# Kernel tuning notes

Hardware: AMD Instinct MI355X
Metric: run time of the kernel (lower is better)

The kernel has to match this reference:

```python
import math
import jax, jax.numpy as jnp
import numpy as np

B, H, HKV, L, S, D = 1, 32, 8, 2048, 2048, 128
N_REP = H // HKV          # 4
SCALE = 1.0 / math.sqrt(D)


def setup_inputs() -> dict:
    key = jax.random.key(0)
    k1, k2, k3, k4 = jax.random.split(key, 4)
    query = jax.random.normal(k1, (B, H, L, D), dtype=jnp.float32)
    k_ = jax.random.normal(k2, (B, HKV, S, D), dtype=jnp.float32)
    v_ = jax.random.normal(k3, (B, HKV, S, D), dtype=jnp.float32)
    attn_mask = jax.random.normal(k4, (B, 1, L, S), dtype=jnp.float32)
    return {"query": query, "key": k_, "value": v_, "attn_mask": attn_mask}


def reference(query, key, value, attn_mask):
    # repeat_kv: Q -> [B, HKV, n_rep, L, D]; K/V stay [B, HKV, S, D]
    # (the torch code reshapes K/V to [B, HKV, 1, S, D]; broadcasting via
    # einsum is equivalent), mask unsqueezed at dim 1 -> [B, 1, 1, L, S].
    q = query.reshape(B, HKV, N_REP, L, D)
    scores = jnp.einsum("bkrld,bksd->bkrls", q, key)          # [B,HKV,n_rep,L,S]
    scores = scores + attn_mask[:, None]                        # broadcast add
    # softmax_fp8(x, dim=-1, invAttnHead=1/sqrt(D)) scales input by invAttnHead
    w = jax.nn.softmax(scores * SCALE, axis=-1)
    # dropout_p = 0.0 -> identity
    out = jnp.einsum("bkrls,bksd->bkrld", w, value)             # [B,HKV,n_rep,L,D]
    return out
```

## Files before the change

### kernel.cpp

```cpp
#include <hip/hip_runtime.h>

#define NH   32
#define NKV  8
#define LQ   2048
#define SK   2048
#define DH   128
#define BM   128
#define BN   64
#define NT   (SK / BN)
#define VSTRIDE 72

typedef __attribute__((ext_vector_type(8)))  short bf8;
typedef __attribute__((ext_vector_type(16))) float f16v;
typedef __attribute__((ext_vector_type(4)))  unsigned int u32x4;

#define CL2E 0.12754308753f

#if __has_builtin(__builtin_amdgcn_exp2f)
#define EXP2F(x) __builtin_amdgcn_exp2f(x)
#else
#define EXP2F(x) exp2f(x)
#endif

__device__ __forceinline__ unsigned short f2bf(float f) {
    unsigned int u = __builtin_bit_cast(unsigned int, f);
    u = (u + 0x7FFFu + ((u >> 16) & 1u)) >> 16;
    return (unsigned short)u;
}

__device__ __forceinline__ unsigned int cvtpk_bf16(float lo, float hi) {
    unsigned int r;
    asm("v_cvt_pk_bf16_f32 %0, %1, %2" : "=v"(r) : "v"(lo), "v"(hi));
    return r;
}

__device__ __forceinline__ float bflo(unsigned int u) {
    return __builtin_bit_cast(float, u << 16);
}
__device__ __forceinline__ float bfhi(unsigned int u) {
    return __builtin_bit_cast(float, u & 0xFFFF0000u);
}

#define GLOAD_LDS16(g, l)                                                      \
    __builtin_amdgcn_global_load_lds(                                          \
        (const __attribute__((address_space(1))) void*)(g),                    \
        (__attribute__((address_space(3))) void*)(l), 16, 0, 0)

__global__ __launch_bounds__(256) void convert_k_kernel(
    const float* __restrict__ K, unsigned short* __restrict__ Kb)
{
    unsigned int cid = blockIdx.x * 256 + threadIdx.x;
    unsigned int p   = cid & 15;
    unsigned int row = cid >> 4;
    unsigned int s   = row & (SK - 1);
    unsigned int c   = p ^ (s & 15);
    const float* src = K + (size_t)row * DH + c * 8;
    float4 a = *(const float4*)(src);
    float4 b = *(const float4*)(src + 4);
    bf8 o;
    o[0] = (short)f2bf(a.x); o[1] = (short)f2bf(a.y);
    o[2] = (short)f2bf(a.z); o[3] = (short)f2bf(a.w);
    o[4] = (short)f2bf(b.x); o[5] = (short)f2bf(b.y);
    o[6] = (short)f2bf(b.z); o[7] = (short)f2bf(b.w);
    *(bf8*)(Kb + (size_t)row * DH + p * 8) = o;
}

__global__ __launch_bounds__(256) void transpose_v_kernel(
    const float* __restrict__ V, unsigned short* __restrict__ VTb)
{
    __shared__ __align__(16) unsigned short Vl[DH * VSTRIDE];
    const int tid = threadIdx.x;
    const int kv  = blockIdx.x >> 5;
    const int t   = blockIdx.x & 31;
    const int s0  = t * 64;
    const float* Vh = V + (size_t)kv * SK * DH;

    #pragma unroll
    for (int i = 0; i < 8; ++i) {
        int idx = tid * 4 + i * 1024;
        int s = idx >> 7, d = idx & 127;
        const float4 v4 = *(const float4*)(Vh + (size_t)(s0 + s) * DH + d);
        Vl[(d + 0) * VSTRIDE + s] = f2bf(v4.x);
        Vl[(d + 1) * VSTRIDE + s] = f2bf(v4.y);
        Vl[(d + 2) * VSTRIDE + s] = f2bf(v4.z);
        Vl[(d + 3) * VSTRIDE + s] = f2bf(v4.w);
    }
    __syncthreads();
    unsigned short* out = VTb + (size_t)(kv * 32 + t) * (DH * 64);
    #pragma unroll
    for (int i = 0; i < 4; ++i) {
        int c = tid + i * 256;
        int d = c >> 3, p = c & 7;
        int sc = (p ^ (d & 7)) * 8;
        *(bf8*)(out + d * 64 + p * 8) = *(const bf8*)(Vl + d * VSTRIDE + sc);
    }
}

__global__ __launch_bounds__(256) void convert_m_kernel(
    const float* __restrict__ M, unsigned short* __restrict__ Mb)
{
    unsigned int cid = blockIdx.x * 256 + threadIdx.x;
    unsigned int row = cid >> 8;
    unsigned int l   = (cid & 255) * 8;
    unsigned int T   = l & ~63u;
    unsigned int loc = l & 63;
    unsigned int mt = loc >> 5, w = loc & 31;
    unsigned int hh = w >> 4, g0 = (w >> 2) & 3;
    const float* src = M + (size_t)row * SK + T + mt * 32 + hh * 4;
    float4 a = *(const float4*)(src + g0 * 8);
    float4 b = *(const float4*)(src + (g0 + 1) * 8);
    bf8 o;
    o[0] = (short)f2bf(a.x * CL2E); o[1] = (short)f2bf(a.y * CL2E);
    o[2] = (short)f2bf(a.z * CL2E); o[3] = (short)f2bf(a.w * CL2E);
    o[4] = (short)f2bf(b.x * CL2E); o[5] = (short)f2bf(b.y * CL2E);
    o[6] = (short)f2bf(b.z * CL2E); o[7] = (short)f2bf(b.w * CL2E);
    *(bf8*)(Mb + (size_t)row * SK + l) = o;
}

__global__ __launch_bounds__(256, 2) void fattn_kernel(
    const float* __restrict__ Q, const unsigned short* __restrict__ Kb,
    const unsigned short* __restrict__ VTb, const unsigned short* __restrict__ Mb,
    float* __restrict__ O)
{
    __shared__ __align__(1024) unsigned char smem[65536];
    unsigned char* KB = smem;
    unsigned char* VB = smem + 32768;

    const int tid  = threadIdx.x;
    const int wave = tid >> 6;
    const int lane = tid & 63;
    const int l32  = lane & 31;
    const int hh   = lane >> 5;

    const int bx = ((int)blockIdx.x & 7) * 64 + ((int)blockIdx.x >> 3);
    const int h  = bx >> 4;
    const int lt = bx & 15;
    const int q0 = lt * BM;
    const int kv = h >> 2;

    const float* Qh = Q + (size_t)h * LQ * DH;
    const unsigned char* Kg = (const unsigned char*)(Kb  + (size_t)kv * SK * DH);
    const unsigned char* Vg = (const unsigned char*)(VTb + (size_t)kv * SK * DH);

    const int qrow = q0 + wave * 32 + l32;
    const unsigned short* Mq = Mb + (size_t)qrow * SK + hh * 16;

    bf8 bQ[8];
    {
        const float* qp = Qh + (size_t)qrow * DH + hh * 8;
        #pragma unroll
        for (int ks = 0; ks < 8; ++ks) {
            float4 a = *(const float4*)(qp + ks * 16);
            float4 b = *(const float4*)(qp + ks * 16 + 4);
            bf8 o;
            o[0] = (short)f2bf(a.x); o[1] = (short)f2bf(a.y);
            o[2] = (short)f2bf(a.z); o[3] = (short)f2bf(a.w);
            o[4] = (short)f2bf(b.x); o[5] = (short)f2bf(b.y);
            o[6] = (short)f2bf(b.z); o[7] = (short)f2bf(b.w);
            bQ[ks] = o;
        }
    }

    const int krow0 = l32 * 256 + ((hh * 16) ^ ((l32 & 15) << 4));
    const int vrowz = l32 * 128 + ((hh * 16) ^ ((l32 & 7) << 4));

    const int stoff = wave * 4096 + lane * 16;

    f16v accO[4];
    #pragma unroll
    for (int dt = 0; dt < 4; ++dt)
        #pragma unroll
        for (int r = 0; r < 16; ++r) accO[dt][r] = 0.f;
    float lpart = 0.f;

    #pragma unroll
    for (int c = 0; c < 4; ++c) GLOAD_LDS16(Kg + stoff + c * 1024, KB + stoff + c * 1024);
    #pragma unroll
    for (int c = 0; c < 4; ++c) GLOAD_LDS16(Vg + stoff + c * 1024, VB + stoff + c * 1024);

    for (int t = 0; t < NT; ++t) {
        const int cur = t & 1;

        const unsigned short* mp = Mq + t * 64;
        u32x4 mA0 = *(const u32x4*)(mp);
        u32x4 mB0 = *(const u32x4*)(mp + 8);
        u32x4 mA1 = *(const u32x4*)(mp + 32);
        u32x4 mB1 = *(const u32x4*)(mp + 40);
        __builtin_amdgcn_sched_barrier(0);

        {
            const int tn = (t + 1) & (NT - 1);
            const unsigned char* ksrc = Kg + (size_t)tn * 16384 + stoff;
            const unsigned char* vsrc = Vg + (size_t)tn * 16384 + stoff;
            unsigned char* kdst = KB + (cur ^ 1) * 16384 + stoff;
            unsigned char* vdst = VB + (cur ^ 1) * 16384 + stoff;
            #pragma unroll
            for (int c = 0; c < 4; ++c) GLOAD_LDS16(ksrc + c * 1024, kdst + c * 1024);
            #pragma unroll
            for (int c = 0; c < 4; ++c) GLOAD_LDS16(vsrc + c * 1024, vdst + c * 1024);
        }
        __builtin_amdgcn_sched_barrier(0);
        asm volatile("s_waitcnt vmcnt(12)" ::: "memory");
        __builtin_amdgcn_s_barrier();
        asm volatile("" ::: "memory");

        const unsigned char* kb = KB + cur * 16384;
        const unsigned char* vb = VB + cur * 16384;

        unsigned int pk0[8], pk1[8];
        #pragma unroll
        for (int mt = 0; mt < 2; ++mt) {
            f16v s;
            #pragma unroll
            for (int r = 0; r < 16; ++r) s[r] = 0.f;
            __builtin_amdgcn_s_setprio(1);
            #pragma unroll
            for (int ks = 0; ks < 8; ++ks) {
                bf8 aK = *(const bf8*)(kb + mt * 8192 + (krow0 ^ (ks << 5)));
                s = __builtin_amdgcn_mfma_f32_32x32x16_bf16(aK, bQ[ks], s, 0, 0, 0);
            }
            __builtin_amdgcn_s_setprio(0);
            const u32x4 mA = mt ? mA1 : mA0;
            const u32x4 mB = mt ? mB1 : mB0;
            unsigned int* pk = mt ? pk1 : pk0;
            #pragma unroll
            for (int g = 0; g < 4; ++g) {
                unsigned int u0 = (g < 2) ? mA[g * 2 + 0] : mB[(g - 2) * 2 + 0];
                unsigned int u1 = (g < 2) ? mA[g * 2 + 1] : mB[(g - 2) * 2 + 1];
                float e0 = EXP2F(fmaf(s[g*4+0], CL2E, bflo(u0)));
                float e1 = EXP2F(fmaf(s[g*4+1], CL2E, bfhi(u0)));
                float e2 = EXP2F(fmaf(s[g*4+2], CL2E, bflo(u1)));
                float e3 = EXP2F(fmaf(s[g*4+3], CL2E, bfhi(u1)));
                lpart += (e0 + e1) + (e2 + e3);
                pk[g*2+0] = cvtpk_bf16(e0, e1);
                pk[g*2+1] = cvtpk_bf16(e2, e3);
            }
        }

        bf8 bP[4];
        #pragma unroll
        for (int ks = 0; ks < 4; ++ks) {
            unsigned int* pk = (ks >> 1) ? pk1 : pk0;
            const int kk = ks & 1;
            unsigned int a0 = pk[kk*4+0], b0 = pk[kk*4+2];
            unsigned int a1 = pk[kk*4+1], b1 = pk[kk*4+3];
            asm volatile("v_permlane32_swap_b32 %0, %1" : "+v"(a0), "+v"(b0));
            asm volatile("v_permlane32_swap_b32 %0, %1" : "+v"(a1), "+v"(b1));
            u32x4 w; w[0] = a0; w[1] = a1; w[2] = b0; w[3] = b1;
            bP[ks] = __builtin_bit_cast(bf8, w);
        }

        __builtin_amdgcn_s_setprio(1);
        #pragma unroll
        for (int dt = 0; dt < 4; ++dt) {
            #pragma unroll
            for (int ks = 0; ks < 4; ++ks) {
                bf8 aV = *(const bf8*)(vb + dt * 4096 + (vrowz ^ (ks << 5)));
                accO[dt] = __builtin_amdgcn_mfma_f32_32x32x16_bf16(aV, bP[ks], accO[dt], 0, 0, 0);
            }
        }
        __builtin_amdgcn_s_setprio(0);
        asm volatile("" ::: "memory");
        __builtin_amdgcn_s_barrier();
        asm volatile("" ::: "memory");
    }

    asm volatile("s_waitcnt vmcnt(0)" ::: "memory");
    float l = lpart + __shfl_xor(lpart, 32);
    float inv = 1.0f / l;
    float* Op = O + (size_t)h * LQ * DH + (size_t)qrow * DH;
    #pragma unroll
    for (int dt = 0; dt < 4; ++dt) {
        #pragma unroll
        for (int g = 0; g < 4; ++g) {
            int d = dt * 32 + g * 8 + hh * 4;
            float4 o;
            o.x = accO[dt][g * 4 + 0] * inv;
            o.y = accO[dt][g * 4 + 1] * inv;
            o.z = accO[dt][g * 4 + 2] * inv;
            o.w = accO[dt][g * 4 + 3] * inv;
            *(float4*)(Op + d) = o;
        }
    }
}

extern "C" void kernel_launch(void* const* d_in, const int* in_sizes, int n_in,
                              void* d_out, int out_size, void* d_ws, size_t ws_size,
                              hipStream_t stream) {
    const float* Q = (const float*)d_in[0];
    const float* K = (const float*)d_in[1];
    const float* V = (const float*)d_in[2];
    const float* M = (const float*)d_in[3];
    float* O = (float*)d_out;

    unsigned short* Kb  = (unsigned short*)d_ws;
    unsigned short* VTb = Kb + (size_t)NKV * SK * DH;
    unsigned short* Mb  = VTb + (size_t)NKV * DH * SK;

    convert_k_kernel<<<dim3((NKV * SK * 16) / 256), 256, 0, stream>>>(K, Kb);
    transpose_v_kernel<<<dim3(NKV * (SK / 64)), 256, 0, stream>>>(V, VTb);
    convert_m_kernel<<<dim3((LQ * (SK / 8)) / 256), 256, 0, stream>>>(M, Mb);

    dim3 grid(NH * (LQ / BM));
    fattn_kernel<<<grid, 256, 0, stream>>>(Q, Kb, VTb, Mb, O);
}
```

Measured before the change: 185.1 us.

## Software-pipeline QK^T one tile ahead of PV and merge prep kernels

The three preprocessing kernels (K convert, V transpose, mask convert) are merged into one launch that dispatches on block index, removing two kernel launches. The attention main loop is restructured so the QK^T MFMAs for tile t+1 are issued while the softmax and PV for tile t proceed. K is prefetched two tiles ahead and V one tile ahead, using ping-pong score registers and a 2x unrolled loop. This is meant to overlap exp/convert work with matrix ops and hide LDS latency, at the cost of more live VGPRs (two extra 16-float score accumulators). The explicit vmcnt waits are replaced by __syncthreads, so correctness now relies on __syncthreads also waiting for the outstanding global-to-LDS loads.

```diff
diff --git a/kernel.cpp b/kernel.cpp
--- a/kernel.cpp
+++ b/kernel.cpp
@@ -46,76 +46,162 @@
         (const __attribute__((address_space(1))) void*)(g),                    \
         (__attribute__((address_space(3))) void*)(l), 16, 0, 0)
 
-__global__ __launch_bounds__(256) void convert_k_kernel(
-    const float* __restrict__ K, unsigned short* __restrict__ Kb)
-{
-    unsigned int cid = blockIdx.x * 256 + threadIdx.x;
-    unsigned int p   = cid & 15;
-    unsigned int row = cid >> 4;
-    unsigned int s   = row & (SK - 1);
-    unsigned int c   = p ^ (s & 15);
-    const float* src = K + (size_t)row * DH + c * 8;
-    float4 a = *(const float4*)(src);
-    float4 b = *(const float4*)(src + 4);
-    bf8 o;
-    o[0] = (short)f2bf(a.x); o[1] = (short)f2bf(a.y);
-    o[2] = (short)f2bf(a.z); o[3] = (short)f2bf(a.w);
-    o[4] = (short)f2bf(b.x); o[5] = (short)f2bf(b.y);
-    o[6] = (short)f2bf(b.z); o[7] = (short)f2bf(b.w);
-    *(bf8*)(Kb + (size_t)row * DH + p * 8) = o;
-}
-
-__global__ __launch_bounds__(256) void transpose_v_kernel(
-    const float* __restrict__ V, unsigned short* __restrict__ VTb)
+__global__ __launch_bounds__(256) void prep_kernel(
+    const float* __restrict__ K, unsigned short* __restrict__ Kb,
+    const float* __restrict__ V, unsigned short* __restrict__ VTb,
+    const float* __restrict__ M, unsigned short* __restrict__ Mb)
 {
     __shared__ __align__(16) unsigned short Vl[DH * VSTRIDE];
     const int tid = threadIdx.x;
-    const int kv  = blockIdx.x >> 5;
-    const int t   = blockIdx.x & 31;
-    const int s0  = t * 64;
-    const float* Vh = V + (size_t)kv * SK * DH;
-
-    #pragma unroll
-    for (int i = 0; i < 8; ++i) {
-        int idx = tid * 4 + i * 1024;
-        int s = idx >> 7, d = idx & 127;
-        const float4 v4 = *(const float4*)(Vh + (size_t)(s0 + s) * DH + d);
-        Vl[(d + 0) * VSTRIDE + s] = f2bf(v4.x);
-        Vl[(d + 1) * VSTRIDE + s] = f2bf(v4.y);
-        Vl[(d + 2) * VSTRIDE + s] = f2bf(v4.z);
-        Vl[(d + 3) * VSTRIDE + s] = f2bf(v4.w);
-    }
-    __syncthreads();
-    unsigned short* out = VTb + (size_t)(kv * 32 + t) * (DH * 64);
-    #pragma unroll
-    for (int i = 0; i < 4; ++i) {
-        int c = tid + i * 256;
-        int d = c >> 3, p = c & 7;
-        int sc = (p ^ (d & 7)) * 8;
-        *(bf8*)(out + d * 64 + p * 8) = *(const bf8*)(Vl + d * VSTRIDE + sc);
-    }
-}
-
-__global__ __launch_bounds__(256) void convert_m_kernel(
-    const float* __restrict__ M, unsigned short* __restrict__ Mb)
-{
-    unsigned int cid = blockIdx.x * 256 + threadIdx.x;
-    unsigned int row = cid >> 8;
-    unsigned int l   = (cid & 255) * 8;
-    unsigned int T   = l & ~63u;
-    unsigned int loc = l & 63;
-    unsigned int mt = loc >> 5, w = loc & 31;
-    unsigned int hh = w >> 4, g0 = (w >> 2) & 3;
-    const float* src = M + (size_t)row * SK + T + mt * 32 + hh * 4;
-    float4 a = *(const float4*)(src + g0 * 8);
-    float4 b = *(const float4*)(src + (g0 + 1) * 8);
-    bf8 o;
-    o[0] = (short)f2bf(a.x * CL2E); o[1] = (short)f2bf(a.y * CL2E);
-    o[2] = (short)f2bf(a.z * CL2E); o[3] = (short)f2bf(a.w * CL2E);
-    o[4] = (short)f2bf(b.x * CL2E); o[5] = (short)f2bf(b.y * CL2E);
-    o[6] = (short)f2bf(b.z * CL2E); o[7] = (short)f2bf(b.w * CL2E);
-    *(bf8*)(Mb + (size_t)row * SK + l) = o;
-}
+    const int bid = blockIdx.x;
+
+    if (bid < 1024) {
+        unsigned int cid = bid * 256 + tid;
+        unsigned int p   = cid & 15;
+        unsigned int row = cid >> 4;
+        unsigned int s   = row & (SK - 1);
+        unsigned int c   = p ^ (s & 15);
+        const float* src = K + (size_t)row * DH + c * 8;
+        float4 a = *(const float4*)(src);
+        float4 b = *(const float4*)(src + 4);
+        bf8 o;
+        o[0] = (short)f2bf(a.x); o[1] = (short)f2bf(a.y);
+        o[2] = (short)f2bf(a.z); o[3] = (short)f2bf(a.w);
+        o[4] = (short)f2bf(b.x); o[5] = (short)f2bf(b.y);
+        o[6] = (short)f2bf(b.z); o[7] = (short)f2bf(b.w);
+        *(bf8*)(Kb + (size_t)row * DH + p * 8) = o;
+    } else if (bid < 1280) {
+        const int vb = bid - 1024;
+        const int kv = vb >> 5;
+        const int t  = vb & 31;
+        const int s0 = t * 64;
+        const float* Vh = V + (size_t)kv * SK * DH;
+        #pragma unroll
+        for (int i = 0; i < 8; ++i) {
+            int idx = tid * 4 + i * 1024;
+            int s = idx >> 7, d = idx & 127;
+            const float4 v4 = *(const float4*)(Vh + (size_t)(s0 + s) * DH + d);
+            Vl[(d + 0) * VSTRIDE + s] = f2bf(v4.x);
+            Vl[(d + 1) * VSTRIDE + s] = f2bf(v4.y);
+            Vl[(d + 2) * VSTRIDE + s] = f2bf(v4.z);
+            Vl[(d + 3) * VSTRIDE + s] = f2bf(v4.w);
+        }
+        __syncthreads();
+        unsigned short* out = VTb + (size_t)(kv * 32 + t) * (DH * 64);
+        #pragma unroll
+        for (int i = 0; i < 4; ++i) {
+            int c = tid + i * 256;
+            int d = c >> 3, p = c & 7;
+            int sc = (p ^ (d & 7)) * 8;
+            *(bf8*)(out + d * 64 + p * 8) = *(const bf8*)(Vl + d * VSTRIDE + sc);
+        }
+    } else {
+        unsigned int cid = (bid - 1280) * 256 + tid;
+        unsigned int row = cid >> 8;
+        unsigned int l   = (cid & 255) * 8;
+        unsigned int T   = l & ~63u;
+        unsigned int loc = l & 63;
+        unsigned int mt = loc >> 5, w = loc & 31;
+        unsigned int hh = w >> 4, g0 = (w >> 2) & 3;
+        const float* src = M + (size_t)row * SK + T + mt * 32 + hh * 4;
+        float4 a = *(const float4*)(src + g0 * 8);
+        float4 b = *(const float4*)(src + (g0 + 1) * 8);
+        bf8 o;
+        o[0] = (short)f2bf(a.x * CL2E); o[1] = (short)f2bf(a.y * CL2E);
+        o[2] = (short)f2bf(a.z * CL2E); o[3] = (short)f2bf(a.w * CL2E);
+        o[4] = (short)f2bf(b.x * CL2E); o[5] = (short)f2bf(b.y * CL2E);
+        o[6] = (short)f2bf(b.z * CL2E); o[7] = (short)f2bf(b.w * CL2E);
+        *(bf8*)(Mb + (size_t)row * SK + l) = o;
+    }
+}
+
+#define BODY(T, CUR, SC0, SC1, SN0, SN1)                                       \
+  {                                                                            \
+    __syncthreads();                                                           \
+    const unsigned short* mp = Mq + (T) * 64;                                  \
+    u32x4 mA0 = *(const u32x4*)(mp);                                           \
+    u32x4 mB0 = *(const u32x4*)(mp + 8);                                       \
+    u32x4 mA1 = *(const u32x4*)(mp + 32);                                      \
+    u32x4 mB1 = *(const u32x4*)(mp + 40);                                      \
+    {                                                                          \
+      const int tv = ((T) + 1) & (NT - 1);                                     \
+      const int tk = ((T) + 2) & (NT - 1);                                     \
+      const unsigned char* vsrc = Vg + (size_t)tv * 16384 + stoff;             \
+      const unsigned char* ksrc = Kg + (size_t)tk * 16384 + stoff;             \
+      unsigned char* vdst = VB + ((CUR) ^ 1) * 16384 + stoff;                  \
+      unsigned char* kdst = KB + (CUR) * 16384 + stoff;                        \
+      _Pragma("unroll")                                                        \
+      for (int c = 0; c < 4; ++c) GLOAD_LDS16(vsrc + c * 1024, vdst + c * 1024); \
+      _Pragma("unroll")                                                        \
+      for (int c = 0; c < 4; ++c) GLOAD_LDS16(ksrc + c * 1024, kdst + c * 1024); \
+    }                                                                          \
+    __builtin_amdgcn_sched_barrier(0);                                         \
+    const unsigned char* kbn = KB + ((CUR) ^ 1) * 16384;                       \
+    const unsigned char* vbc = VB + (CUR) * 16384;                             \
+    _Pragma("unroll")                                                          \
+    for (int r = 0; r < 16; ++r) { SN0[r] = 0.f; SN1[r] = 0.f; }               \
+    __builtin_amdgcn_s_setprio(1);                                             \
+    _Pragma("unroll")                                                          \
+    for (int ks = 0; ks < 8; ++ks) {                                           \
+      bf8 aK = *(const bf8*)(kbn + (krow0 ^ (ks << 5)));                       \
+      SN0 = __builtin_amdgcn_mfma_f32_32x32x16_bf16(aK, bQ[ks], SN0, 0, 0, 0); \
+    }                                                                          \
+    __builtin_amdgcn_s_setprio(0);                                             \
+    unsigned int pk0[8], pk1[8];                                               \
+    _Pragma("unroll")                                                          \
+    for (int g = 0; g < 4; ++g) {                                              \
+      unsigned int u0 = (g < 2) ? mA0[g * 2 + 0] : mB0[(g - 2) * 2 + 0];       \
+      unsigned int u1 = (g < 2) ? mA0[g * 2 + 1] : mB0[(g - 2) * 2 + 1];       \
+      float e0 = EXP2F(fmaf(SC0[g*4+0], CL2E, bflo(u0)));                      \
+      float e1 = EXP2F(fmaf(SC0[g*4+1], CL2E, bfhi(u0)));                      \
+      float e2 = EXP2F(fmaf(SC0[g*4+2], CL2E, bflo(u1)));                      \
+      float e3 = EXP2F(fmaf(SC0[g*4+3], CL2E, bfhi(u1)));                      \
+      lpA += (e0 + e1) + (e2 + e3);                                            \
+      pk0[g*2+0] = cvtpk_bf16(e0, e1);                                         \
+      pk0[g*2+1] = cvtpk_bf16(e2, e3);                                         \
+    }                                                                          \
+    __builtin_amdgcn_s_setprio(1);                                             \
+    _Pragma("unroll")                                                          \
+    for (int ks = 0; ks < 8; ++ks) {                                           \
+      bf8 aK = *(const bf8*)(kbn + 8192 + (krow0 ^ (ks << 5)));                \
+      SN1 = __builtin_amdgcn_mfma_f32_32x32x16_bf16(aK, bQ[ks], SN1, 0, 0, 0); \
+    }                                                                          \
+    __builtin_amdgcn_s_setprio(0);                                             \
+    _Pragma("unroll")                                                          \
+    for (int g = 0; g < 4; ++g) {                                              \
+      unsigned int u0 = (g < 2) ? mA1[g * 2 + 0] : mB1[(g - 2) * 2 + 0];       \
+      unsigned int u1 = (g < 2) ? mA1[g * 2 + 1] : mB1[(g - 2) * 2 + 1];       \
+      float e0 = EXP2F(fmaf(SC1[g*4+0], CL2E, bflo(u0)));                      \
+      float e1 = EXP2F(fmaf(SC1[g*4+1], CL2E, bfhi(u0)));                      \
+      float e2 = EXP2F(fmaf(SC1[g*4+2], CL2E, bflo(u1)));                      \
+      float e3 = EXP2F(fmaf(SC1[g*4+3], CL2E, bfhi(u1)));                      \
+      lpB += (e0 + e1) + (e2 + e3);                                            \
+      pk1[g*2+0] = cvtpk_bf16(e0, e1);                                         \
+      pk1[g*2+1] = cvtpk_bf16(e2, e3);                                         \
+    }                                                                          \
+    bf8 bP[4];                                                                 \
+    _Pragma("unroll")                                                          \
+    for (int ks = 0; ks < 4; ++ks) {                                           \
+      unsigned int* pk = (ks >> 1) ? pk1 : pk0;                                \
+      const int kk = ks & 1;                                                   \
+      unsigned int a0 = pk[kk*4+0], b0 = pk[kk*4+2];                           \
+      unsigned int a1 = pk[kk*4+1], b1 = pk[kk*4+3];                           \
+      asm volatile("v_permlane32_swap_b32 %0, %1" : "+v"(a0), "+v"(b0));       \
+      asm volatile("v_permlane32_swap_b32 %0, %1" : "+v"(a1), "+v"(b1));       \
+      u32x4 w; w[0] = a0; w[1] = a1; w[2] = b0; w[3] = b1;                     \
+      bP[ks] = __builtin_bit_cast(bf8, w);                                     \
+    }                                                                          \
+    __builtin_amdgcn_s_setprio(1);                                             \
+    _Pragma("unroll")                                                          \
+    for (int dt = 0; dt < 4; ++dt) {                                           \
+      _Pragma("unroll")                                                        \
+      for (int ks = 0; ks < 4; ++ks) {                                         \
+        bf8 aV = *(const bf8*)(vbc + dt * 4096 + (vrowz ^ (ks << 5)));         \
+        accO[dt] = __builtin_amdgcn_mfma_f32_32x32x16_bf16(aV, bP[ks], accO[dt], 0, 0, 0); \
+      }                                                                        \
+    }                                                                          \
+    __builtin_amdgcn_s_setprio(0);                                             \
+  }
 
 __global__ __launch_bounds__(256, 2) void fattn_kernel(
     const float* __restrict__ Q, const unsigned short* __restrict__ Kb,
@@ -171,101 +257,39 @@
     for (int dt = 0; dt < 4; ++dt)
         #pragma unroll
         for (int r = 0; r < 16; ++r) accO[dt][r] = 0.f;
-    float lpart = 0.f;
+    float lpA = 0.f, lpB = 0.f;
 
     #pragma unroll
     for (int c = 0; c < 4; ++c) GLOAD_LDS16(Kg + stoff + c * 1024, KB + stoff + c * 1024);
     #pragma unroll
     for (int c = 0; c < 4; ++c) GLOAD_LDS16(Vg + stoff + c * 1024, VB + stoff + c * 1024);
-
-    for (int t = 0; t < NT; ++t) {
-        const int cur = t & 1;
-
-        const unsigned short* mp = Mq + t * 64;
-        u32x4 mA0 = *(const u32x4*)(mp);
-        u32x4 mB0 = *(const u32x4*)(mp + 8);
-        u32x4 mA1 = *(const u32x4*)(mp + 32);
-        u32x4 mB1 = *(const u32x4*)(mp + 40);
-        __builtin_amdgcn_sched_barrier(0);
-
-        {
-            const int tn = (t + 1) & (NT - 1);
-            const unsigned char* ksrc = Kg + (size_t)tn * 16384 + stoff;
-            const unsigned char* vsrc = Vg + (size_t)tn * 16384 + stoff;
-            unsigned char* kdst = KB + (cur ^ 1) * 16384 + stoff;
-            unsigned char* vdst = VB + (cur ^ 1) * 16384 + stoff;
-            #pragma unroll
-            for (int c = 0; c < 4; ++c) GLOAD_LDS16(ksrc + c * 1024, kdst + c * 1024);
-            #pragma unroll
-            for (int c = 0; c < 4; ++c) GLOAD_LDS16(vsrc + c * 1024, vdst + c * 1024);
-        }
-        __builtin_amdgcn_sched_barrier(0);
-        asm volatile("s_waitcnt vmcnt(12)" ::: "memory");
-        __builtin_amdgcn_s_barrier();
-        asm volatile("" ::: "memory");
-
-        const unsigned char* kb = KB + cur * 16384;
-        const unsigned char* vb = VB + cur * 16384;
-
-        unsigned int pk0[8], pk1[8];
-        #pragma unroll
-        for (int mt = 0; mt < 2; ++mt) {
-            f16v s;
-            #pragma unroll
-            for (int r = 0; r < 16; ++r) s[r] = 0.f;
-            __builtin_amdgcn_s_setprio(1);
-            #pragma unroll
-            for (int ks = 0; ks < 8; ++ks) {
-                bf8 aK = *(const bf8*)(kb + mt * 8192 + (krow0 ^ (ks << 5)));
-                s = __builtin_amdgcn_mfma_f32_32x32x16_bf16(aK, bQ[ks], s, 0, 0, 0);
-            }
-            __builtin_amdgcn_s_setprio(0);
-            const u32x4 mA = mt ? mA1 : mA0;
-            const u32x4 mB = mt ? mB1 : mB0;
-            unsigned int* pk = mt ? pk1 : pk0;
-            #pragma unroll
-            for (int g = 0; g < 4; ++g) {
-                unsigned int u0 = (g < 2) ? mA[g * 2 + 0] : mB[(g - 2) * 2 + 0];
-                unsigned int u1 = (g < 2) ? mA[g * 2 + 1] : mB[(g - 2) * 2 + 1];
-                float e0 = EXP2F(fmaf(s[g*4+0], CL2E, bflo(u0)));
-                float e1 = EXP2F(fmaf(s[g*4+1], CL2E, bfhi(u0)));
-                float e2 = EXP2F(fmaf(s[g*4+2], CL2E, bflo(u1)));
-                float e3 = EXP2F(fmaf(s[g*4+3], CL2E, bfhi(u1)));
-                lpart += (e0 + e1) + (e2 + e3);
-                pk[g*2+0] = cvtpk_bf16(e0, e1);
-                pk[g*2+1] = cvtpk_bf16(e2, e3);
-            }
-        }
-
-        bf8 bP[4];
-        #pragma unroll
-        for (int ks = 0; ks < 4; ++ks) {
-            unsigned int* pk = (ks >> 1) ? pk1 : pk0;
-            const int kk = ks & 1;
-            unsigned int a0 = pk[kk*4+0], b0 = pk[kk*4+2];
-            unsigned int a1 = pk[kk*4+1], b1 = pk[kk*4+3];
-            asm volatile("v_permlane32_swap_b32 %0, %1" : "+v"(a0), "+v"(b0));
-            asm volatile("v_permlane32_swap_b32 %0, %1" : "+v"(a1), "+v"(b1));
-            u32x4 w; w[0] = a0; w[1] = a1; w[2] = b0; w[3] = b1;
-            bP[ks] = __builtin_bit_cast(bf8, w);
-        }
-
-        __builtin_amdgcn_s_setprio(1);
-        #pragma unroll
-        for (int dt = 0; dt < 4; ++dt) {
-            #pragma unroll
-            for (int ks = 0; ks < 4; ++ks) {
-                bf8 aV = *(const bf8*)(vb + dt * 4096 + (vrowz ^ (ks << 5)));
-                accO[dt] = __builtin_amdgcn_mfma_f32_32x32x16_bf16(aV, bP[ks], accO[dt], 0, 0, 0);
-            }
-        }
-        __builtin_amdgcn_s_setprio(0);
-        asm volatile("" ::: "memory");
-        __builtin_amdgcn_s_barrier();
-        asm volatile("" ::: "memory");
+    #pragma unroll
+    for (int c = 0; c < 4; ++c) GLOAD_LDS16(Kg + 16384 + stoff + c * 1024, KB + 16384 + stoff + c * 1024);
+    __syncthreads();
+
+    f16v sA0, sA1, sB0, sB1;
+    #pragma unroll
+    for (int r = 0; r < 16; ++r) { sA0[r] = 0.f; sA1[r] = 0.f; }
+    __builtin_amdgcn_s_setprio(1);
+    #pragma unroll
+    for (int ks = 0; ks < 8; ++ks) {
+        bf8 aK = *(const bf8*)(KB + (krow0 ^ (ks << 5)));
+        sA0 = __builtin_amdgcn_mfma_f32_32x32x16_bf16(aK, bQ[ks], sA0, 0, 0, 0);
+    }
+    #pragma unroll
+    for (int ks = 0; ks < 8; ++ks) {
+        bf8 aK = *(const bf8*)(KB + 8192 + (krow0 ^ (ks << 5)));
+        sA1 = __builtin_amdgcn_mfma_f32_32x32x16_bf16(aK, bQ[ks], sA1, 0, 0, 0);
+    }
+    __builtin_amdgcn_s_setprio(0);
+
+    for (int tt = 0; tt < NT; tt += 2) {
+        BODY(tt + 0, 0, sA0, sA1, sB0, sB1)
+        BODY(tt + 1, 1, sB0, sB1, sA0, sA1)
     }
 
     asm volatile("s_waitcnt vmcnt(0)" ::: "memory");
+    float lpart = lpA + lpB;
     float l = lpart + __shfl_xor(lpart, 32);
     float inv = 1.0f / l;
     float* Op = O + (size_t)h * LQ * DH + (size_t)qrow * DH;
@@ -297,9 +321,7 @@
     unsigned short* VTb = Kb + (size_t)NKV * SK * DH;
     unsigned short* Mb  = VTb + (size_t)NKV * DH * SK;
 
-    convert_k_kernel<<<dim3((NKV * SK * 16) / 256), 256, 0, stream>>>(K, Kb);
-    transpose_v_kernel<<<dim3(NKV * (SK / 64)), 256, 0, stream>>>(V, VTb);
-    convert_m_kernel<<<dim3((LQ * (SK / 8)) / 256), 256, 0, stream>>>(M, Mb);
+    prep_kernel<<<dim3(3328), 256, 0, stream>>>(K, Kb, V, VTb, M, Mb);
 
     dim3 grid(NH * (LQ / BM));
     fattn_kernel<<<grid, 256, 0, stream>>>(Q, Kb, VTb, Mb, O);
```

New measurement: 179.6 us. 1.03x faster.

## Double query tile per block to reuse K/V LDS reads; merge prep kernels

Applied to the files above, without the earlier changes.

Each wave now handles two 32-row query tiles (BM 256), so every K and V fragment read from LDS feeds two MFMAs instead of one. This halves the grid to 256 blocks with a single-block-per-CU launch bound. The per-iteration barrier logic is replaced by a __syncthreads at loop start. The three preprocessing kernels (K convert, V transpose, mask convert) are fused into one launch to cut launch overhead. The trade-off is one wave per SIMD, which leaves less latency hiding for the per-thread mask loads and the exp work, plus higher register pressure.

```diff
diff --git a/kernel.cpp b/kernel.cpp
--- a/kernel.cpp
+++ b/kernel.cpp
@@ -5,7 +5,7 @@
 #define LQ   2048
 #define SK   2048
 #define DH   128
-#define BM   128
+#define BM   256
 #define BN   64
 #define NT   (SK / BN)
 #define VSTRIDE 72
@@ -46,78 +46,76 @@
         (const __attribute__((address_space(1))) void*)(g),                    \
         (__attribute__((address_space(3))) void*)(l), 16, 0, 0)
 
-__global__ __launch_bounds__(256) void convert_k_kernel(
-    const float* __restrict__ K, unsigned short* __restrict__ Kb)
-{
-    unsigned int cid = blockIdx.x * 256 + threadIdx.x;
-    unsigned int p   = cid & 15;
-    unsigned int row = cid >> 4;
-    unsigned int s   = row & (SK - 1);
-    unsigned int c   = p ^ (s & 15);
-    const float* src = K + (size_t)row * DH + c * 8;
-    float4 a = *(const float4*)(src);
-    float4 b = *(const float4*)(src + 4);
-    bf8 o;
-    o[0] = (short)f2bf(a.x); o[1] = (short)f2bf(a.y);
-    o[2] = (short)f2bf(a.z); o[3] = (short)f2bf(a.w);
-    o[4] = (short)f2bf(b.x); o[5] = (short)f2bf(b.y);
-    o[6] = (short)f2bf(b.z); o[7] = (short)f2bf(b.w);
-    *(bf8*)(Kb + (size_t)row * DH + p * 8) = o;
-}
-
-__global__ __launch_bounds__(256) void transpose_v_kernel(
-    const float* __restrict__ V, unsigned short* __restrict__ VTb)
+__global__ __launch_bounds__(256) void prep_kernel(
+    const float* __restrict__ K, unsigned short* __restrict__ Kb,
+    const float* __restrict__ V, unsigned short* __restrict__ VTb,
+    const float* __restrict__ M, unsigned short* __restrict__ Mb)
 {
     __shared__ __align__(16) unsigned short Vl[DH * VSTRIDE];
     const int tid = threadIdx.x;
-    const int kv  = blockIdx.x >> 5;
-    const int t   = blockIdx.x & 31;
-    const int s0  = t * 64;
-    const float* Vh = V + (size_t)kv * SK * DH;
-
-    #pragma unroll
-    for (int i = 0; i < 8; ++i) {
-        int idx = tid * 4 + i * 1024;
-        int s = idx >> 7, d = idx & 127;
-        const float4 v4 = *(const float4*)(Vh + (size_t)(s0 + s) * DH + d);
-        Vl[(d + 0) * VSTRIDE + s] = f2bf(v4.x);
-        Vl[(d + 1) * VSTRIDE + s] = f2bf(v4.y);
-        Vl[(d + 2) * VSTRIDE + s] = f2bf(v4.z);
-        Vl[(d + 3) * VSTRIDE + s] = f2bf(v4.w);
+    const int bid = blockIdx.x;
+
+    if (bid < 1024) {
+        unsigned int cid = bid * 256 + tid;
+        unsigned int p   = cid & 15;
+        unsigned int row = cid >> 4;
+        unsigned int s   = row & (SK - 1);
+        unsigned int c   = p ^ (s & 15);
+        const float* src = K + (size_t)row * DH + c * 8;
+        float4 a = *(const float4*)(src);
+        float4 b = *(const float4*)(src + 4);
+        bf8 o;
+        o[0] = (short)f2bf(a.x); o[1] = (short)f2bf(a.y);
+        o[2] = (short)f2bf(a.z); o[3] = (short)f2bf(a.w);
+        o[4] = (short)f2bf(b.x); o[5] = (short)f2bf(b.y);
+        o[6] = (short)f2bf(b.z); o[7] = (short)f2bf(b.w);
+        *(bf8*)(Kb + (size_t)row * DH + p * 8) = o;
+    } else if (bid < 1280) {
+        const int vb = bid - 1024;
+        const int kv = vb >> 5;
+        const int t  = vb & 31;
+        const int s0 = t * 64;
+        const float* Vh = V + (size_t)kv * SK * DH;
+        #pragma unroll
+        for (int i = 0; i < 8; ++i) {
+            int idx = tid * 4 + i * 1024;
+            int s = idx >> 7, d = idx & 127;
+            const float4 v4 = *(const float4*)(Vh + (size_t)(s0 + s) * DH + d);
+            Vl[(d + 0) * VSTRIDE + s] = f2bf(v4.x);
+            Vl[(d + 1) * VSTRIDE + s] = f2bf(v4.y);
+            Vl[(d + 2) * VSTRIDE + s] = f2bf(v4.z);
+            Vl[(d + 3) * VSTRIDE + s] = f2bf(v4.w);
+        }
+        __syncthreads();
+        unsigned short* out = VTb + (size_t)(kv * 32 + t) * (DH * 64);
+        #pragma unroll
+        for (int i = 0; i < 4; ++i) {
+            int c = tid + i * 256;
+            int d = c >> 3, p = c & 7;
+            int sc = (p ^ (d & 7)) * 8;
+            *(bf8*)(out + d * 64 + p * 8) = *(const bf8*)(Vl + d * VSTRIDE + sc);
+        }
+    } else {
+        unsigned int cid = (bid - 1280) * 256 + tid;
+        unsigned int row = cid >> 8;
+        unsigned int l   = (cid & 255) * 8;
+        unsigned int T   = l & ~63u;
+        unsigned int loc = l & 63;
+        unsigned int mt = loc >> 5, w = loc & 31;
+        unsigned int hh = w >> 4, g0 = (w >> 2) & 3;
+        const float* src = M + (size_t)row * SK + T + mt * 32 + hh * 4;
+        float4 a = *(const float4*)(src + g0 * 8);
+        float4 b = *(const float4*)(src + (g0 + 1) * 8);
+        bf8 o;
+        o[0] = (short)f2bf(a.x * CL2E); o[1] = (short)f2bf(a.y * CL2E);
+        o[2] = (short)f2bf(a.z * CL2E); o[3] = (short)f2bf(a.w * CL2E);
+        o[4] = (short)f2bf(b.x * CL2E); o[5] = (short)f2bf(b.y * CL2E);
+        o[6] = (short)f2bf(b.z * CL2E); o[7] = (short)f2bf(b.w * CL2E);
+        *(bf8*)(Mb + (size_t)row * SK + l) = o;
     }
-    __syncthreads();
-    unsigned short* out = VTb + (size_t)(kv * 32 + t) * (DH * 64);
-    #pragma unroll
-    for (int i = 0; i < 4; ++i) {
-        int c = tid + i * 256;
-        int d = c >> 3, p = c & 7;
-        int sc = (p ^ (d & 7)) * 8;
-        *(bf8*)(out + d * 64 + p * 8) = *(const bf8*)(Vl + d * VSTRIDE + sc);
-    }
-}
-
-__global__ __launch_bounds__(256) void convert_m_kernel(
-    const float* __restrict__ M, unsigned short* __restrict__ Mb)
-{
-    unsigned int cid = blockIdx.x * 256 + threadIdx.x;
-    unsigned int row = cid >> 8;
-    unsigned int l   = (cid & 255) * 8;
-    unsigned int T   = l & ~63u;
-    unsigned int loc = l & 63;
-    unsigned int mt = loc >> 5, w = loc & 31;
-    unsigned int hh = w >> 4, g0 = (w >> 2) & 3;
-    const float* src = M + (size_t)row * SK + T + mt * 32 + hh * 4;
-    float4 a = *(const float4*)(src + g0 * 8);
-    float4 b = *(const float4*)(src + (g0 + 1) * 8);
-    bf8 o;
-    o[0] = (short)f2bf(a.x * CL2E); o[1] = (short)f2bf(a.y * CL2E);
-    o[2] = (short)f2bf(a.z * CL2E); o[3] = (short)f2bf(a.w * CL2E);
-    o[4] = (short)f2bf(b.x * CL2E); o[5] = (short)f2bf(b.y * CL2E);
-    o[6] = (short)f2bf(b.z * CL2E); o[7] = (short)f2bf(b.w * CL2E);
-    *(bf8*)(Mb + (size_t)row * SK + l) = o;
-}
-
-__global__ __launch_bounds__(256, 2) void fattn_kernel(
+}
+
+__global__ __launch_bounds__(256, 1) void fattn_kernel(
     const float* __restrict__ Q, const unsigned short* __restrict__ Kb,
     const unsigned short* __restrict__ VTb, const unsigned short* __restrict__ Mb,
     float* __restrict__ O)
@@ -132,9 +130,9 @@
     const int l32  = lane & 31;
     const int hh   = lane >> 5;
 
-    const int bx = ((int)blockIdx.x & 7) * 64 + ((int)blockIdx.x >> 3);
-    const int h  = bx >> 4;
-    const int lt = bx & 15;
+    const int bx = ((int)blockIdx.x & 7) * 32 + ((int)blockIdx.x >> 3);
+    const int h  = bx >> 3;
+    const int lt = bx & 7;
     const int q0 = lt * BM;
     const int kv = h >> 2;
 
@@ -142,12 +140,14 @@
     const unsigned char* Kg = (const unsigned char*)(Kb  + (size_t)kv * SK * DH);
     const unsigned char* Vg = (const unsigned char*)(VTb + (size_t)kv * SK * DH);
 
-    const int qrow = q0 + wave * 32 + l32;
-    const unsigned short* Mq = Mb + (size_t)qrow * SK + hh * 16;
-
-    bf8 bQ[8];
-    {
-        const float* qp = Qh + (size_t)qrow * DH + hh * 8;
+    const int qrow0 = q0 + wave * 64 + l32;
+    const unsigned short* Mq0 = Mb + (size_t)qrow0 * SK + hh * 16;
+    const unsigned short* Mq1 = Mq0 + (size_t)32 * SK;
+
+    bf8 bQ[2][8];
+    #pragma unroll
+    for (int qt = 0; qt < 2; ++qt) {
+        const float* qp = Qh + (size_t)(qrow0 + qt * 32) * DH + hh * 8;
         #pragma unroll
         for (int ks = 0; ks < 8; ++ks) {
             float4 a = *(const float4*)(qp + ks * 16);
@@ -157,7 +157,7 @@
             o[2] = (short)f2bf(a.z); o[3] = (short)f2bf(a.w);
             o[4] = (short)f2bf(b.x); o[5] = (short)f2bf(b.y);
             o[6] = (short)f2bf(b.z); o[7] = (short)f2bf(b.w);
-            bQ[ks] = o;
+            bQ[qt][ks] = o;
         }
     }
 
@@ -166,12 +166,14 @@
 
     const int stoff = wave * 4096 + lane * 16;
 
-    f16v accO[4];
+    f16v accO[4][2];
     #pragma unroll
     for (int dt = 0; dt < 4; ++dt)
         #pragma unroll
-        for (int r = 0; r < 16; ++r) accO[dt][r] = 0.f;
-    float lpart = 0.f;
+        for (int qt = 0; qt < 2; ++qt)
+            #pragma unroll
+            for (int r = 0; r < 16; ++r) accO[dt][qt][r] = 0.f;
+    float lp0 = 0.f, lp1 = 0.f;
 
     #pragma unroll
     for (int c = 0; c < 4; ++c) GLOAD_LDS16(Kg + stoff + c * 1024, KB + stoff + c * 1024);
@@ -180,13 +182,18 @@
 
     for (int t = 0; t < NT; ++t) {
         const int cur = t & 1;
-
-        const unsigned short* mp = Mq + t * 64;
-        u32x4 mA0 = *(const u32x4*)(mp);
-        u32x4 mB0 = *(const u32x4*)(mp + 8);
-        u32x4 mA1 = *(const u32x4*)(mp + 32);
-        u32x4 mB1 = *(const u32x4*)(mp + 40);
-        __builtin_amdgcn_sched_barrier(0);
+        __syncthreads();
+
+        const unsigned short* mp0 = Mq0 + t * 64;
+        const unsigned short* mp1 = Mq1 + t * 64;
+        u32x4 mA00 = *(const u32x4*)(mp0);
+        u32x4 mB00 = *(const u32x4*)(mp0 + 8);
+        u32x4 mA01 = *(const u32x4*)(mp0 + 32);
+        u32x4 mB01 = *(const u32x4*)(mp0 + 40);
+        u32x4 mA10 = *(const u32x4*)(mp1);
+        u32x4 mB10 = *(const u32x4*)(mp1 + 8);
+        u32x4 mA11 = *(const u32x4*)(mp1 + 32);
+        u32x4 mB11 = *(const u32x4*)(mp1 + 40);
 
         {
             const int tn = (t + 1) & (NT - 1);
@@ -200,54 +207,108 @@
             for (int c = 0; c < 4; ++c) GLOAD_LDS16(vsrc + c * 1024, vdst + c * 1024);
         }
         __builtin_amdgcn_sched_barrier(0);
-        asm volatile("s_waitcnt vmcnt(12)" ::: "memory");
-        __builtin_amdgcn_s_barrier();
-        asm volatile("" ::: "memory");
 
         const unsigned char* kb = KB + cur * 16384;
         const unsigned char* vb = VB + cur * 16384;
 
-        unsigned int pk0[8], pk1[8];
-        #pragma unroll
-        for (int mt = 0; mt < 2; ++mt) {
-            f16v s;
-            #pragma unroll
-            for (int r = 0; r < 16; ++r) s[r] = 0.f;
-            __builtin_amdgcn_s_setprio(1);
-            #pragma unroll
-            for (int ks = 0; ks < 8; ++ks) {
-                bf8 aK = *(const bf8*)(kb + mt * 8192 + (krow0 ^ (ks << 5)));
-                s = __builtin_amdgcn_mfma_f32_32x32x16_bf16(aK, bQ[ks], s, 0, 0, 0);
+        f16v s0a, s0b;
+        #pragma unroll
+        for (int r = 0; r < 16; ++r) { s0a[r] = 0.f; s0b[r] = 0.f; }
+        __builtin_amdgcn_s_setprio(1);
+        #pragma unroll
+        for (int ks = 0; ks < 8; ++ks) {
+            bf8 aK = *(const bf8*)(kb + (krow0 ^ (ks << 5)));
+            s0a = __builtin_amdgcn_mfma_f32_32x32x16_bf16(aK, bQ[0][ks], s0a, 0, 0, 0);
+            s0b = __builtin_amdgcn_mfma_f32_32x32x16_bf16(aK, bQ[1][ks], s0b, 0, 0, 0);
+        }
+        __builtin_amdgcn_s_setprio(0);
+
+        unsigned int pk00[8], pk10[8];
+        #pragma unroll
+        for (int g = 0; g < 4; ++g) {
+            unsigned int u0 = (g < 2) ? mA00[g * 2 + 0] : mB00[(g - 2) * 2 + 0];
+            unsigned int u1 = (g < 2) ? mA00[g * 2 + 1] : mB00[(g - 2) * 2 + 1];
+            float e0 = EXP2F(fmaf(s0a[g*4+0], CL2E, bflo(u0)));
+            float e1 = EXP2F(fmaf(s0a[g*4+1], CL2E, bfhi(u0)));
+            float e2 = EXP2F(fmaf(s0a[g*4+2], CL2E, bflo(u1)));
+            float e3 = EXP2F(fmaf(s0a[g*4+3], CL2E, bfhi(u1)));
+            lp0 += (e0 + e1) + (e2 + e3);
+            pk00[g*2+0] = cvtpk_bf16(e0, e1);
+            pk00[g*2+1] = cvtpk_bf16(e2, e3);
+        }
+        #pragma unroll
+        for (int g = 0; g < 4; ++g) {
+            unsigned int u0 = (g < 2) ? mA10[g * 2 + 0] : mB10[(g - 2) * 2 + 0];
+            unsigned int u1 = (g < 2) ? mA10[g * 2 + 1] : mB10[(g - 2) * 2 + 1];
+            float e0 = EXP2F(fmaf(s0b[g*4+0], CL2E, bflo(u0)));
+            float e1 = EXP2F(fmaf(s0b[g*4+1], CL2E, bfhi(u0)));
+            float e2 = EXP2F(fmaf(s0b[g*4+2], CL2E, bflo(u1)));
+            float e3 = EXP2F(fmaf(s0b[g*4+3], CL2E, bfhi(u1)));
+            lp1 += (e0 + e1) + (e2 + e3);
+            pk10[g*2+0] = cvtpk_bf16(e0, e1);
+            pk10[g*2+1] = cvtpk_bf16(e2, e3);
+        }
+
+        f16v s1a, s1b;
+        #pragma unroll
+        for (int r = 0; r < 16; ++r) { s1a[r] = 0.f; s1b[r] = 0.f; }
+        __builtin_amdgcn_s_setprio(1);
+        #pragma unroll
+        for (int ks = 0; ks < 8; ++ks) {
+            bf8 aK = *(const bf8*)(kb + 8192 + (krow0 ^ (ks << 5)));
+            s1a = __builtin_amdgcn_mfma_f32_32x32x16_bf16(aK, bQ[0][ks], s1a, 0, 0, 0);
+            s1b = __builtin_amdgcn_mfma_f32_32x32x16_bf16(aK, bQ[1][ks], s1b, 0, 0, 0);
+        }
+        __builtin_amdgcn_s_setprio(0);
+
+        unsigned int pk01[8], pk11[8];
+        #pragma unroll
+        for (int g = 0; g < 4; ++g) {
+            unsigned int u0 = (g < 2) ? mA01[g * 2 + 0] : mB01[(g - 2) * 2 + 0];
+            unsigned int u1 = (g < 2) ? mA01[g * 2 + 1] : mB01[(g - 2) * 2 + 1];
+            float e0 = EXP2F(fmaf(s1a[g*4+0], CL2E, bflo(u0)));
+            float e1 = EXP2F(fmaf(s1a[g*4+1], CL2E, bfhi(u0)));
+            float e2 = EXP2F(fmaf(s1a[g*4+2], CL2E, bflo(u1)));
+            float e3 = EXP2F(fmaf(s1a[g*4+3], CL2E, bfhi(u1)));
+            lp0 += (e0 + e1) + (e2 + e3);
+            pk01[g*2+0] = cvtpk_bf16(e0, e1);
+            pk01[g*2+1] = cvtpk_bf16(e2, e3);
+        }
+        #pragma unroll
+        for (int g = 0; g < 4; ++g) {
+            unsigned int u0 = (g < 2) ? mA11[g * 2 + 0] : mB11[(g - 2) * 2 + 0];
+            unsigned int u1 = (g < 2) ? mA11[g * 2 + 1] : mB11[(g - 2) * 2 + 1];
+            float e0 = EXP2F(fmaf(s1b[g*4+0], CL2E, bflo(u0)));
+            float e1 = EXP2F(fmaf(s1b[g*4+1], CL2E, bfhi(u0)));
+            float e2 = EXP2F(fmaf(s1b[g*4+2], CL2E, bflo(u1)));
+            float e3 = EXP2F(fmaf(s1b[g*4+3], CL2E, bfhi(u1)));
+            lp1 += (e0 + e1) + (e2 + e3);
+            pk11[g*2+0] = cvtpk_bf16(e0, e1);
+            pk11[g*2+1] = cvtpk_bf16(e2, e3);
+        }
+
+        bf8 bP0[4], bP1[4];
+        #pragma unroll
+        for (int ks = 0; ks < 4; ++ks) {
+            const int kk = ks & 1;
+            {
+                unsigned int* pk = (ks >> 1) ? pk01 : pk00;
+                unsigned int a0 = pk[kk*4+0], b0 = pk[kk*4+2];
+                unsigned int a1 = pk[kk*4+1], b1 = pk[kk*4+3];
+                asm volatile("v_permlane32_swap_b32 %0, %1" : "+v"(a0), "+v"(b0));
+                asm volatile("v_permlane32_swap_b32 %0, %1" : "+v"(a1), "+v"(b1));
+                u32x4 w; w[0] = a0; w[1] = a1; w[2] = b0; w[3] = b1;
+                bP0[ks] = __builtin_bit_cast(bf8, w);
             }
-            __builtin_amdgcn_s_setprio(0);
-            const u32x4 mA = mt ? mA1 : mA0;
-            const u32x4 mB = mt ? mB1 : mB0;
-            unsigned int* pk = mt ? pk1 : pk0;
-            #pragma unroll
-            for (int g = 0; g < 4; ++g) {
-                unsigned int u0 = (g < 2) ? mA[g * 2 + 0] : mB[(g - 2) * 2 + 0];
-                unsigned int u1 = (g < 2) ? mA[g * 2 + 1] : mB[(g - 2) * 2 + 1];
-                float e0 = EXP2F(fmaf(s[g*4+0], CL2E, bflo(u0)));
-                float e1 = EXP2F(fmaf(s[g*4+1], CL2E, bfhi(u0)));
-                float e2 = EXP2F(fmaf(s[g*4+2], CL2E, bflo(u1)));
-                float e3 = EXP2F(fmaf(s[g*4+3], CL2E, bfhi(u1)));
-                lpart += (e0 + e1) + (e2 + e3);
-                pk[g*2+0] = cvtpk_bf16(e0, e1);
-                pk[g*2+1] = cvtpk_bf16(e2, e3);
+            {
+                unsigned int* pk = (ks >> 1) ? pk11 : pk10;
+                unsigned int a0 = pk[kk*4+0], b0 = pk[kk*4+2];
+                unsigned int a1 = pk[kk*4+1], b1 = pk[kk*4+3];
+                asm volatile("v_permlane32_swap_b32 %0, %1" : "+v"(a0), "+v"(b0));
+                asm volatile("v_permlane32_swap_b32 %0, %1" : "+v"(a1), "+v"(b1));
+                u32x4 w; w[0] = a0; w[1] = a1; w[2] = b0; w[3] = b1;
+                bP1[ks] = __builtin_bit_cast(bf8, w);
             }
-        }
-
-        bf8 bP[4];
-        #pragma unroll
-        for (int ks = 0; ks < 4; ++ks) {
-            unsigned int* pk = (ks >> 1) ? pk1 : pk0;
-            const int kk = ks & 1;
-            unsigned int a0 = pk[kk*4+0], b0 = pk[kk*4+2];
-            unsigned int a1 = pk[kk*4+1], b1 = pk[kk*4+3];
-            asm volatile("v_permlane32_swap_b32 %0, %1" : "+v"(a0), "+v"(b0));
-            asm volatile("v_permlane32_swap_b32 %0, %1" : "+v"(a1), "+v"(b1));
-            u32x4 w; w[0] = a0; w[1] = a1; w[2] = b0; w[3] = b1;
-            bP[ks] = __builtin_bit_cast(bf8, w);
         }
 
         __builtin_amdgcn_s_setprio(1);
@@ -256,30 +317,35 @@
             #pragma unroll
             for (int ks = 0; ks < 4; ++ks) {
                 bf8 aV = *(const bf8*)(vb + dt * 4096 + (vrowz ^ (ks << 5)));
-                accO[dt] = __builtin_amdgcn_mfma_f32_32x32x16_bf16(aV, bP[ks], accO[dt], 0, 0, 0);
+                accO[dt][0] = __builtin_amdgcn_mfma_f32_32x32x16_bf16(aV, bP0[ks], accO[dt][0], 0, 0, 0);
+                accO[dt][1] = __builtin_amdgcn_mfma_f32_32x32x16_bf16(aV, bP1[ks], accO[dt][1], 0, 0, 0);
             }
         }
         __builtin_amdgcn_s_setprio(0);
-        asm volatile("" ::: "memory");
-        __builtin_amdgcn_s_barrier();
-        asm volatile("" ::: "memory");
     }
 
     asm volatile("s_waitcnt vmcnt(0)" ::: "memory");
-    float l = lpart + __shfl_xor(lpart, 32);
-    float inv = 1.0f / l;
-    float* Op = O + (size_t)h * LQ * DH + (size_t)qrow * DH;
-    #pragma unroll
-    for (int dt = 0; dt < 4; ++dt) {
-        #pragma unroll
-        for (int g = 0; g < 4; ++g) {
-            int d = dt * 32 + g * 8 + hh * 4;
-            float4 o;
-            o.x = accO[dt][g * 4 + 0] * inv;
-            o.y = accO[dt][g * 4 + 1] * inv;
-            o.z = accO[dt][g * 4 + 2] * inv;
-            o.w = accO[dt][g * 4 + 3] * inv;
-            *(float4*)(Op + d) = o;
+    float l0 = lp0 + __shfl_xor(lp0, 32);
+    float l1 = lp1 + __shfl_xor(lp1, 32);
+    const float inv0 = 1.0f / l0;
+    const float inv1 = 1.0f / l1;
+    float* Op0 = O + (size_t)h * LQ * DH + (size_t)qrow0 * DH;
+    #pragma unroll
+    for (int qt = 0; qt < 2; ++qt) {
+        const float inv = qt ? inv1 : inv0;
+        float* Op = Op0 + (size_t)qt * 32 * DH;
+        #pragma unroll
+        for (int dt = 0; dt < 4; ++dt) {
+            #pragma unroll
+            for (int g = 0; g < 4; ++g) {
+                int d = dt * 32 + g * 8 + hh * 4;
+                float4 o;
+                o.x = accO[dt][qt][g * 4 + 0] * inv;
+                o.y = accO[dt][qt][g * 4 + 1] * inv;
+                o.z = accO[dt][qt][g * 4 + 2] * inv;
+                o.w = accO[dt][qt][g * 4 + 3] * inv;
+                *(float4*)(Op + d) = o;
+            }
         }
     }
 }
@@ -297,9 +363,7 @@
     unsigned short* VTb = Kb + (size_t)NKV * SK * DH;
     unsigned short* Mb  = VTb + (size_t)NKV * DH * SK;
 
-    convert_k_kernel<<<dim3((NKV * SK * 16) / 256), 256, 0, stream>>>(K, Kb);
-    transpose_v_kernel<<<dim3(NKV * (SK / 64)), 256, 0, stream>>>(V, VTb);
-    convert_m_kernel<<<dim3((LQ * (SK / 8)) / 256), 256, 0, stream>>>(M, Mb);
+    prep_kernel<<<dim3(3328), 256, 0, stream>>>(K, Kb, V, VTb, M, Mb);
 
     dim3 grid(NH * (LQ / BM));
     fattn_kernel<<<grid, 256, 0, stream>>>(Q, Kb, VTb, Mb, O);
```

Measured after the change: 215.5 us. +16.4%, slower.
